# Performance work log

Measured on AMD Instinct MI355X. Metric: run time of the kernel, lower is better.

The kernel has to match this reference:

```python
import jax, jax.numpy as jnp
import numpy as np

D_IN = 1024
N_HEADS = 16
DEPTH = D_IN // N_HEADS
SCALE = float(np.sqrt(DEPTH))


def setup_inputs() -> dict:
    key = jax.random.key(0)
    ks = jax.random.split(key, 11)
    B, S = 4, 1024
    s = 0.02
    return {
        "q": jax.random.normal(ks[0], (B, S, D_IN), jnp.float32),
        "k": jax.random.normal(ks[1], (B, S, D_IN), jnp.float32),
        "v": jax.random.normal(ks[2], (B, S, D_IN), jnp.float32),
        "mask": jnp.zeros((1, 1, S, S), jnp.float32),
        "wq_w": jax.random.normal(ks[3], (D_IN, D_IN), jnp.float32) * s,
        "wq_b": jax.random.normal(ks[4], (D_IN,), jnp.float32) * s,
        "wk_w": jax.random.normal(ks[5], (D_IN, D_IN), jnp.float32) * s,
        "wk_b": jax.random.normal(ks[6], (D_IN,), jnp.float32) * s,
        "wv_w": jax.random.normal(ks[7], (D_IN, D_IN), jnp.float32) * s,
        "wv_b": jax.random.normal(ks[8], (D_IN,), jnp.float32) * s,
        "pl_w": jax.random.normal(ks[9], (D_IN, D_IN), jnp.float32) * s,
        "pl_b": jax.random.normal(ks[10], (D_IN,), jnp.float32) * s,
    }


def _split_heads(x):
    # [B, S, D] -> [B, H, S, depth]
    B, S, _ = x.shape
    return x.reshape(B, S, N_HEADS, DEPTH).transpose(0, 2, 1, 3)


def reference(q, k, v, mask, wq_w, wq_b, wk_w, wk_b, wv_w, wv_b, pl_w, pl_b):
    # torch Linear: y = x @ W.T + b
    qh = _split_heads(q @ wq_w.T + wq_b)
    kh = _split_heads(k @ wk_w.T + wk_b)
    vh = _split_heads(v @ wv_w.T + wv_b)
    # [B, H, Sq, Sk]
    logits = jnp.einsum("bhqd,bhkd->bhqk", qh, kh) / SCALE
    logits = logits + mask * (-1e9)
    weights = jax.nn.softmax(logits, axis=-1)
    attn = jnp.einsum("bhqk,bhkd->bhqd", weights, vh)
    B = q.shape[0]
    attn = attn.transpose(0, 2, 1, 3).reshape(B, -1, D_IN)
    return attn @ pl_w.T + pl_b
```

## Files before the change

### kernel.cpp

```cpp
#include <hip/hip_runtime.h>
#include <stdint.h>

#define B_ 4
#define S_ 1024
#define DMODEL 1024
#define H_ 16
#define DP_ 64

typedef __attribute__((ext_vector_type(8))) short short8;
typedef __attribute__((ext_vector_type(4))) float floatx4;
typedef __attribute__((ext_vector_type(16))) float floatx16;
typedef __attribute__((ext_vector_type(8))) unsigned short ushort8;
typedef __attribute__((ext_vector_type(4))) unsigned short ushort4v;

#define LOG2E 1.44269504088896f

__device__ __forceinline__ unsigned short f2bf(float x) {
    union { float f; unsigned int u; } c; c.f = x;
    unsigned int r = c.u + 0x7FFFu + ((c.u >> 16) & 1u);
    return (unsigned short)(r >> 16);
}
__device__ __forceinline__ unsigned short f2bf_fast(float x) {
    union { float f; unsigned int u; } c; c.f = x;
    return (unsigned short)((c.u + 0x8000u) >> 16);
}
__device__ __forceinline__ float bf2f(unsigned short b) {
    union { float f; unsigned int u; } c; c.u = ((unsigned int)b) << 16;
    return c.f;
}

#if __has_builtin(__builtin_amdgcn_exp2f)
#define EXP2(x) __builtin_amdgcn_exp2f(x)
#else
#define EXP2(x) exp2f(x)
#endif

#define GLDS16(gp, lp) __builtin_amdgcn_global_load_lds( \
    (const __attribute__((address_space(1))) void*)(gp),  \
    (__attribute__((address_space(3))) void*)(lp), 16, 0, 0)

__global__ __launch_bounds__(256) void convert_all(
    const float* __restrict__ q, const float* __restrict__ k, const float* __restrict__ v,
    const float* __restrict__ wq, const float* __restrict__ wk, const float* __restrict__ wv,
    const float* __restrict__ wp, const float* __restrict__ mask,
    unsigned short* __restrict__ ws)
{
    const unsigned g = blockIdx.x * 256u + threadIdx.x;
    const float* s; unsigned short* d; unsigned off; float sc = 1.0f;
    if (g < 524288u)        { s = q;  d = ws;            off = g; }
    else if (g < 1048576u)  { s = k;  d = ws + 4194304;  off = g - 524288u; }
    else if (g < 1572864u)  { s = v;  d = ws + 8388608;  off = g - 1048576u; }
    else if (g < 1703936u)  { s = wq; d = ws + 12582912; off = g - 1572864u; }
    else if (g < 1835008u)  { s = wk; d = ws + 13631488; off = g - 1703936u; }
    else if (g < 1966080u)  { s = wv; d = ws + 14680064; off = g - 1835008u; }
    else if (g < 2097152u)  { s = wp; d = ws + 15728640; off = g - 1966080u; }
    else { s = mask; d = ws + 16777216; off = g - 2097152u; sc = -1e9f * LOG2E; }
    const floatx4 a = ((const floatx4*)s)[(size_t)off * 2];
    const floatx4 b = ((const floatx4*)s)[(size_t)off * 2 + 1];
    ushort8 r;
    r[0] = f2bf(a[0] * sc); r[1] = f2bf(a[1] * sc); r[2] = f2bf(a[2] * sc); r[3] = f2bf(a[3] * sc);
    r[4] = f2bf(b[0] * sc); r[5] = f2bf(b[1] * sc); r[6] = f2bf(b[2] * sc); r[7] = f2bf(b[3] * sc);
    ((ushort8*)d)[off] = r;
}

template<bool SWAP>
__device__ __forceinline__ void gemm_body(
    const unsigned short* __restrict__ X, const unsigned short* __restrict__ W,
    const int row0, const int col0,
    unsigned short* Xs, unsigned short* Ws, floatx4* acc)
{
    const int tid = threadIdx.x, w = tid >> 6, lane = tid & 63;
    const int l15 = lane & 15, l4 = lane >> 4;
    const int wr = w >> 1, wc = w & 1;
    const int srow = lane >> 3;
    const int sgrp = (lane & 7) ^ srow;
    auto* XsL = (__attribute__((address_space(3))) unsigned short*)Xs;
    auto* WsL = (__attribute__((address_space(3))) unsigned short*)Ws;

    for (int it = 0; it < 16; it++) {
        const int kk = it * 64;
        __syncthreads();
        for (int j = 0; j < 4; j++) {
            const int rb = w * 32 + j * 8;
            GLDS16(X + (size_t)(row0 + rb + srow) * DMODEL + kk + sgrp * 8, XsL + rb * 64);
            GLDS16(W + (size_t)(col0 + rb + srow) * DMODEL + kk + sgrp * 8, WsL + rb * 64);
        }
        __syncthreads();
        for (int ks = 0; ks < 2; ks++) {
            const int slot = ((ks * 4 + l4) ^ (l15 & 7)) * 8;
            short8 xf[4], wf[4];
            for (int t = 0; t < 4; t++) {
                xf[t] = *(const short8*)(Xs + (wr * 64 + t * 16 + l15) * 64 + slot);
                wf[t] = *(const short8*)(Ws + (wc * 64 + t * 16 + l15) * 64 + slot);
            }
            for (int a = 0; a < 4; a++)
                for (int b2 = 0; b2 < 4; b2++)
                    acc[a * 4 + b2] = SWAP
                        ? __builtin_amdgcn_mfma_f32_16x16x32_bf16(wf[a], xf[b2], acc[a * 4 + b2], 0, 0, 0)
                        : __builtin_amdgcn_mfma_f32_16x16x32_bf16(xf[a], wf[b2], acc[a * 4 + b2], 0, 0, 0);
        }
    }
}

__global__ __launch_bounds__(256, 3) void qkv_gemm(
    const unsigned short* __restrict__ Xall, const unsigned short* __restrict__ Wall,
    const float* __restrict__ bq, const float* __restrict__ bk, const float* __restrict__ bv,
    unsigned short* __restrict__ Qh, unsigned short* __restrict__ Kh,
    unsigned short* __restrict__ Vt)
{
    __shared__ unsigned short Xs[8192];
    __shared__ unsigned short Ws[8192];
    const int sel = blockIdx.y >> 5;
    const int row0 = (blockIdx.y & 31) * 128, col0 = blockIdx.x * 128;
    const unsigned short* X = Xall + (size_t)sel * 4194304;
    const unsigned short* W = Wall + (size_t)sel * 1048576;
    const float* bias = (sel == 0) ? bq : (sel == 1) ? bk : bv;

    const int tid = threadIdx.x, w = tid >> 6, lane = tid & 63;
    const int l15 = lane & 15, l4 = lane >> 4;
    const int wr = w >> 1, wc = w & 1;

    floatx4 acc[16];
    for (int i = 0; i < 16; i++) acc[i] = (floatx4){0.f, 0.f, 0.f, 0.f};

    if (sel < 2) {
        gemm_body<true>(X, W, row0, col0, Xs, Ws, acc);
        unsigned short* Out = sel ? Kh : Qh;
        const float scale = sel ? 1.0f : 0.125f * LOG2E;
        for (int nt = 0; nt < 4; nt++) {
            const int n0 = col0 + wc * 64 + nt * 16 + l4 * 4;
            const floatx4 bv4 = *(const floatx4*)(bias + n0);
            const int h = n0 >> 6, d0 = n0 & 63;
            for (int mt = 0; mt < 4; mt++) {
                const int m = row0 + wr * 64 + mt * 16 + l15;
                const int b = m >> 10, s = m & 1023;
                const floatx4 a = acc[nt * 4 + mt];
                ushort4v pk;
                for (int i = 0; i < 4; i++) pk[i] = f2bf((a[i] + bv4[i]) * scale);
                *(ushort4v*)(Out + (((size_t)(b * H_ + h) * S_ + s) * DP_ + d0)) = pk;
            }
        }
    } else {
        gemm_body<false>(X, W, row0, col0, Xs, Ws, acc);
        for (int mt = 0; mt < 4; mt++) {
            const int m0 = row0 + wr * 64 + mt * 16 + l4 * 4;
            const int b = m0 >> 10, s0 = m0 & 1023;
            for (int nt = 0; nt < 4; nt++) {
                const int n = col0 + wc * 64 + nt * 16 + l15;
                const int h = n >> 6, d = n & 63;
                const float bvv = bias[n];
                const floatx4 a = acc[mt * 4 + nt];
                ushort4v pk;
                for (int i = 0; i < 4; i++) pk[i] = f2bf(a[i] + bvv);
                *(ushort4v*)(Vt + (((size_t)(b * H_ + h) * DP_ + d) * S_ + s0)) = pk;
            }
        }
    }
}

__global__ __launch_bounds__(256, 4) void out_gemm(
    const unsigned short* __restrict__ X, const unsigned short* __restrict__ W,
    const float* __restrict__ bias, float* __restrict__ Out)
{
    __shared__ unsigned short Xs[128 * 64];
    __shared__ unsigned short Ws[64 * 64];
    const int row0 = blockIdx.y * 128, col0 = blockIdx.x * 64;
    const int tid = threadIdx.x, w = tid >> 6, lane = tid & 63;
    const int l15 = lane & 15, l4 = lane >> 4;
    const int srow = lane >> 3, sgrp = (lane & 7) ^ srow;
    auto* XsL = (__attribute__((address_space(3))) unsigned short*)Xs;
    auto* WsL = (__attribute__((address_space(3))) unsigned short*)Ws;

    floatx4 acc[8];
    for (int i = 0; i < 8; i++) acc[i] = (floatx4){0.f, 0.f, 0.f, 0.f};

    for (int it = 0; it < 16; it++) {
        const int kk = it * 64;
        __syncthreads();
        for (int j = 0; j < 4; j++) {
            const int rb = w * 32 + j * 8;
            GLDS16(X + (size_t)(row0 + rb + srow) * DMODEL + kk + sgrp * 8, XsL + rb * 64);
        }
        for (int j = 0; j < 2; j++) {
            const int rb = w * 16 + j * 8;
            GLDS16(W + (size_t)(col0 + rb + srow) * DMODEL + kk + sgrp * 8, WsL + rb * 64);
        }
        __syncthreads();
        for (int ks = 0; ks < 2; ks++) {
            const int slot = ((ks * 4 + l4) ^ (l15 & 7)) * 8;
            short8 xf[2], wf[4];
            for (int t = 0; t < 2; t++)
                xf[t] = *(const short8*)(Xs + (w * 32 + t * 16 + l15) * 64 + slot);
            for (int t = 0; t < 4; t++)
                wf[t] = *(const short8*)(Ws + (t * 16 + l15) * 64 + slot);
            for (int nt = 0; nt < 4; nt++)
                for (int mt = 0; mt < 2; mt++)
                    acc[nt * 2 + mt] = __builtin_amdgcn_mfma_f32_16x16x32_bf16(
                        wf[nt], xf[mt], acc[nt * 2 + mt], 0, 0, 0);
        }
    }

    for (int nt = 0; nt < 4; nt++) {
        const int n0 = col0 + nt * 16 + l4 * 4;
        const floatx4 bv4 = *(const floatx4*)(bias + n0);
        for (int mt = 0; mt < 2; mt++) {
            const int m = row0 + w * 32 + mt * 16 + l15;
            floatx4 ov;
            for (int i = 0; i < 4; i++) ov[i] = acc[nt * 2 + mt][i] + bv4[i];
            *(floatx4*)(Out + (size_t)m * DMODEL + n0) = ov;
        }
    }
}

__global__ __launch_bounds__(256, 3) void attn_fwd(
    const unsigned short* __restrict__ Qh, const unsigned short* __restrict__ Kh,
    const unsigned short* __restrict__ Vt, const unsigned short* __restrict__ maskb,
    unsigned short* __restrict__ attnO)
{
    __shared__ unsigned short Ks[2 * 4096];
    __shared__ unsigned short Vs[2 * 4096];
    __shared__ unsigned short Ps[2 * 2048];
    auto* KsL = (__attribute__((address_space(3))) unsigned short*)Ks;
    auto* VsL = (__attribute__((address_space(3))) unsigned short*)Vs;

    const int bh = blockIdx.x, qt = blockIdx.y;
    const int b = bh >> 4, h = bh & 15;
    const int tid = threadIdx.x, w = tid >> 6, lane = tid & 63;
    const int l31 = lane & 31, hh = lane >> 5;
    const int qh = w >> 1, kh = w & 1;
    const int srow = lane >> 3, sgrp = (lane & 7) ^ srow;
    unsigned short* PsQ = Ps + qh * 2048;
    const int qg = qt * 64 + qh * 32 + l31;
    const int sw7 = l31 & 7;

    short8 bq[4];
    for (int c = 0; c < 4; c++)
        bq[c] = *(const short8*)(Qh + ((size_t)bh * S_ + qg) * DP_ + c * 16 + hh * 8);

    for (int j = 0; j < 2; j++) {
        const int rb = w * 16 + j * 8;
        GLDS16(Kh + ((size_t)bh * S_ + rb + srow) * DP_ + sgrp * 8, KsL + rb * 64);
        GLDS16(Vt + ((size_t)bh * DP_ + rb + srow) * S_ + sgrp * 8, VsL + rb * 64);
    }
    ushort4v mk[4], mkn[4];
    for (int rq = 0; rq < 4; rq++)
        mk[rq] = *(const ushort4v*)(maskb + (size_t)qg * S_ + kh * 32 + rq * 8 + hh * 4);

    float l_i = 0.f;
    floatx16 o;
    for (int i = 0; i < 16; i++) o[i] = 0.f;

    for (int kt = 0; kt < 16; kt++) {
        const int cur = kt & 1, nxt = cur ^ 1;
        __syncthreads();
        if (kt < 15) {
            for (int j = 0; j < 2; j++) {
                const int rb = w * 16 + j * 8;
                GLDS16(Kh + ((size_t)bh * S_ + (kt + 1) * 64 + rb + srow) * DP_ + sgrp * 8,
                       KsL + nxt * 4096 + rb * 64);
            }
            for (int rq = 0; rq < 4; rq++)
                mkn[rq] = *(const ushort4v*)(maskb + (size_t)qg * S_ + (kt + 1) * 64 + kh * 32 + rq * 8 + hh * 4);
        }

        const unsigned short* Kc = Ks + cur * 4096;
        floatx16 sa;
        for (int i = 0; i < 16; i++) sa[i] = 0.f;
        for (int c = 0; c < 4; c++) {
            short8 ak = *(const short8*)(Kc + (kh * 32 + l31) * 64 + ((c * 2 + hh) ^ sw7) * 8);
            sa = __builtin_amdgcn_mfma_f32_32x32x16_bf16(ak, bq[c], sa, 0, 0, 0);
        }

        for (int rq = 0; rq < 4; rq++) {
            ushort4v pk;
            for (int i = 0; i < 4; i++) {
                const float p = EXP2(sa[rq * 4 + i] + bf2f(mk[rq][i]));
                l_i += p;
                pk[i] = f2bf_fast(p);
            }
            *(ushort4v*)(PsQ + l31 * 64 + ((kh * 4 + rq) ^ sw7) * 8 + hh * 4) = pk;
        }
        __syncthreads();
        if (kt < 15) {
            for (int j = 0; j < 2; j++) {
                const int rb = w * 16 + j * 8;
                GLDS16(Vt + ((size_t)bh * DP_ + rb + srow) * S_ + (kt + 1) * 64 + sgrp * 8,
                       VsL + nxt * 4096 + rb * 64);
            }
        }

        const unsigned short* Vc = Vs + cur * 4096;
        for (int c2 = 0; c2 < 4; c2++) {
            short8 av = *(const short8*)(Vc + (kh * 32 + l31) * 64 + ((c2 * 2 + hh) ^ sw7) * 8);
            short8 bp = *(const short8*)(PsQ + l31 * 64 + ((c2 * 2 + hh) ^ sw7) * 8);
            o = __builtin_amdgcn_mfma_f32_32x32x16_bf16(av, bp, o, 0, 0, 0);
        }

        if (kt < 15)
            for (int rq = 0; rq < 4; rq++) mk[rq] = mkn[rq];
    }

    __syncthreads();
    l_i += __shfl_xor(l_i, 32, 64);
    float* Lbuf = (float*)Ks;
    if (lane < 32) Lbuf[w * 32 + l31] = l_i;
    __syncthreads();
    const float inv = 1.0f / (Lbuf[qh * 64 + l31] + Lbuf[qh * 64 + 32 + l31]);

    unsigned short* T = Ks + 1024;
    for (int rq = 0; rq < 4; rq++) {
        ushort4v pk;
        for (int i = 0; i < 4; i++) pk[i] = f2bf(o[rq * 4 + i] * inv);
        const int qq = qh * 32 + l31;
        *(ushort4v*)(T + qq * 64 + ((kh * 4 + rq) ^ sw7) * 8 + hh * 4) = pk;
    }
    __syncthreads();
    const int r = tid >> 2;
    for (int t = 0; t < 2; t++) {
        const int g = (tid & 3) + t * 4;
        ushort8 ov = *(const ushort8*)(T + r * 64 + ((g ^ (r & 7)) * 8));
        *(ushort8*)(attnO + ((size_t)(b * S_ + qt * 64 + r)) * DMODEL + h * DP_ + g * 8) = ov;
    }
}

extern "C" void kernel_launch(void* const* d_in, const int* in_sizes, int n_in,
                              void* d_out, int out_size, void* d_ws, size_t ws_size,
                              hipStream_t stream)
{
    (void)in_sizes; (void)n_in; (void)out_size; (void)ws_size;
    const float* q    = (const float*)d_in[0];
    const float* k    = (const float*)d_in[1];
    const float* v    = (const float*)d_in[2];
    const float* mask = (const float*)d_in[3];
    const float* wq_w = (const float*)d_in[4];
    const float* wq_b = (const float*)d_in[5];
    const float* wk_w = (const float*)d_in[6];
    const float* wk_b = (const float*)d_in[7];
    const float* wv_w = (const float*)d_in[8];
    const float* wv_b = (const float*)d_in[9];
    const float* pl_w = (const float*)d_in[10];
    const float* pl_b = (const float*)d_in[11];

    unsigned short* ws = (unsigned short*)d_ws;
    unsigned short* Xall  = ws;
    unsigned short* Wall  = ws + 12582912;
    unsigned short* Wp    = ws + 15728640;
    unsigned short* maskb = ws + 16777216;
    unsigned short* Qh    = ws + 17825792;
    unsigned short* Kh    = ws + 22020096;
    unsigned short* Vt    = ws + 4194304;
    unsigned short* attnB = ws;

    dim3 bb(256, 1, 1);
    convert_all<<<dim3(8704, 1, 1), bb, 0, stream>>>(q, k, v, wq_w, wk_w, wv_w, pl_w, mask, ws);
    qkv_gemm<<<dim3(8, 96, 1), bb, 0, stream>>>(Xall, Wall, wq_b, wk_b, wv_b, Qh, Kh, Vt);
    attn_fwd<<<dim3(64, 16, 1), bb, 0, stream>>>(Qh, Kh, Vt, maskb, attnB);
    out_gemm<<<dim3(16, 32, 1), bb, 0, stream>>>(attnB, Wp, pl_b, (float*)d_out);
}
```

Baseline: 220.1 us.

## Keep P in registers via lane shuffles and split PV over key halves

The attention kernel stops writing the softmax probabilities to shared memory and reading them back. Each wave packs its P values to bf16 and swaps halves with the partner lane using cross-lane shuffles to build the PV MFMA operand directly. Each wave now computes all 64 output dims over its own 32-key half, and the two key-half partial outputs are combined through shared memory in the epilogue. This removes the Ps buffer and the mid-iteration barrier, moves the V prefetch to the top of the loop, and raises the occupancy hint to 4; the cost is twice the output accumulator registers and an extra reduction step.

```diff
diff --git a/kernel.cpp b/kernel.cpp
--- a/kernel.cpp
+++ b/kernel.cpp
@@ -12,6 +12,7 @@
 typedef __attribute__((ext_vector_type(16))) float floatx16;
 typedef __attribute__((ext_vector_type(8))) unsigned short ushort8;
 typedef __attribute__((ext_vector_type(4))) unsigned short ushort4v;
+typedef __attribute__((ext_vector_type(4))) unsigned int uintx4;
 
 #define LOG2E 1.44269504088896f
 
@@ -20,13 +21,13 @@
     unsigned int r = c.u + 0x7FFFu + ((c.u >> 16) & 1u);
     return (unsigned short)(r >> 16);
 }
-__device__ __forceinline__ unsigned short f2bf_fast(float x) {
-    union { float f; unsigned int u; } c; c.f = x;
-    return (unsigned short)((c.u + 0x8000u) >> 16);
-}
 __device__ __forceinline__ float bf2f(unsigned short b) {
     union { float f; unsigned int u; } c; c.u = ((unsigned int)b) << 16;
     return c.f;
+}
+__device__ __forceinline__ unsigned pack2(float lo, float hi) {
+    union { float f; unsigned int u; } a, b; a.f = lo; b.f = hi;
+    return ((b.u + 0x8000u) & 0xFFFF0000u) | ((a.u + 0x8000u) >> 16);
 }
 
 #if __has_builtin(__builtin_amdgcn_exp2f)
@@ -212,14 +213,13 @@
     }
 }
 
-__global__ __launch_bounds__(256, 3) void attn_fwd(
+__global__ __launch_bounds__(256, 4) void attn_fwd(
     const unsigned short* __restrict__ Qh, const unsigned short* __restrict__ Kh,
     const unsigned short* __restrict__ Vt, const unsigned short* __restrict__ maskb,
     unsigned short* __restrict__ attnO)
 {
     __shared__ unsigned short Ks[2 * 4096];
     __shared__ unsigned short Vs[2 * 4096];
-    __shared__ unsigned short Ps[2 * 2048];
     auto* KsL = (__attribute__((address_space(3))) unsigned short*)Ks;
     auto* VsL = (__attribute__((address_space(3))) unsigned short*)Vs;
 
@@ -229,7 +229,6 @@
     const int l31 = lane & 31, hh = lane >> 5;
     const int qh = w >> 1, kh = w & 1;
     const int srow = lane >> 3, sgrp = (lane & 7) ^ srow;
-    unsigned short* PsQ = Ps + qh * 2048;
     const int qg = qt * 64 + qh * 32 + l31;
     const int sw7 = l31 & 7;
 
@@ -243,12 +242,13 @@
         GLDS16(Vt + ((size_t)bh * DP_ + rb + srow) * S_ + sgrp * 8, VsL + rb * 64);
     }
     ushort4v mk[4], mkn[4];
-    for (int rq = 0; rq < 4; rq++)
-        mk[rq] = *(const ushort4v*)(maskb + (size_t)qg * S_ + kh * 32 + rq * 8 + hh * 4);
+    for (int t = 0; t < 4; t++)
+        mk[t] = *(const ushort4v*)(maskb + (size_t)qg * S_ + kh * 32 + t * 8 + hh * 4);
 
     float l_i = 0.f;
-    floatx16 o;
-    for (int i = 0; i < 16; i++) o[i] = 0.f;
+    floatx16 o[2];
+    for (int du = 0; du < 2; du++)
+        for (int i = 0; i < 16; i++) o[du][i] = 0.f;
 
     for (int kt = 0; kt < 16; kt++) {
         const int cur = kt & 1, nxt = cur ^ 1;
@@ -258,12 +258,15 @@
                 const int rb = w * 16 + j * 8;
                 GLDS16(Kh + ((size_t)bh * S_ + (kt + 1) * 64 + rb + srow) * DP_ + sgrp * 8,
                        KsL + nxt * 4096 + rb * 64);
-            }
-            for (int rq = 0; rq < 4; rq++)
-                mkn[rq] = *(const ushort4v*)(maskb + (size_t)qg * S_ + (kt + 1) * 64 + kh * 32 + rq * 8 + hh * 4);
+                GLDS16(Vt + ((size_t)bh * DP_ + rb + srow) * S_ + (kt + 1) * 64 + sgrp * 8,
+                       VsL + nxt * 4096 + rb * 64);
+            }
+            for (int t = 0; t < 4; t++)
+                mkn[t] = *(const ushort4v*)(maskb + (size_t)qg * S_ + (kt + 1) * 64 + kh * 32 + t * 8 + hh * 4);
         }
 
         const unsigned short* Kc = Ks + cur * 4096;
+        const unsigned short* Vc = Vs + cur * 4096;
         floatx16 sa;
         for (int i = 0; i < 16; i++) sa[i] = 0.f;
         for (int c = 0; c < 4; c++) {
@@ -271,48 +274,71 @@
             sa = __builtin_amdgcn_mfma_f32_32x32x16_bf16(ak, bq[c], sa, 0, 0, 0);
         }
 
-        for (int rq = 0; rq < 4; rq++) {
-            ushort4v pk;
-            for (int i = 0; i < 4; i++) {
-                const float p = EXP2(sa[rq * 4 + i] + bf2f(mk[rq][i]));
-                l_i += p;
-                pk[i] = f2bf_fast(p);
-            }
-            *(ushort4v*)(PsQ + l31 * 64 + ((kh * 4 + rq) ^ sw7) * 8 + hh * 4) = pk;
-        }
-        __syncthreads();
-        if (kt < 15) {
-            for (int j = 0; j < 2; j++) {
-                const int rb = w * 16 + j * 8;
-                GLDS16(Vt + ((size_t)bh * DP_ + rb + srow) * S_ + (kt + 1) * 64 + sgrp * 8,
-                       VsL + nxt * 4096 + rb * 64);
-            }
-        }
-
-        const unsigned short* Vc = Vs + cur * 4096;
-        for (int c2 = 0; c2 < 4; c2++) {
-            short8 av = *(const short8*)(Vc + (kh * 32 + l31) * 64 + ((c2 * 2 + hh) ^ sw7) * 8);
-            short8 bp = *(const short8*)(PsQ + l31 * 64 + ((c2 * 2 + hh) ^ sw7) * 8);
-            o = __builtin_amdgcn_mfma_f32_32x32x16_bf16(av, bp, o, 0, 0, 0);
-        }
+        unsigned pd[8];
+        for (int t = 0; t < 4; t++) {
+            float p0 = EXP2(sa[t * 4 + 0] + bf2f(mk[t][0]));
+            float p1 = EXP2(sa[t * 4 + 1] + bf2f(mk[t][1]));
+            float p2 = EXP2(sa[t * 4 + 2] + bf2f(mk[t][2]));
+            float p3 = EXP2(sa[t * 4 + 3] + bf2f(mk[t][3]));
+            l_i += (p0 + p1) + (p2 + p3);
+            pd[t * 2 + 0] = pack2(p0, p1);
+            pd[t * 2 + 1] = pack2(p2, p3);
+        }
+
+        unsigned snd0 = hh ? pd[0] : pd[2];
+        unsigned snd1 = hh ? pd[1] : pd[3];
+        unsigned snd2 = hh ? pd[4] : pd[6];
+        unsigned snd3 = hh ? pd[5] : pd[7];
+        unsigned r0 = (unsigned)__shfl_xor((int)snd0, 32, 64);
+        unsigned r1 = (unsigned)__shfl_xor((int)snd1, 32, 64);
+        unsigned r2 = (unsigned)__shfl_xor((int)snd2, 32, 64);
+        unsigned r3 = (unsigned)__shfl_xor((int)snd3, 32, 64);
+        uintx4 u0 = { hh ? r0 : pd[0], hh ? r1 : pd[1], hh ? pd[2] : r0, hh ? pd[3] : r1 };
+        uintx4 u1 = { hh ? r2 : pd[4], hh ? r3 : pd[5], hh ? pd[6] : r2, hh ? pd[7] : r3 };
+        short8 bp[2];
+        bp[0] = __builtin_bit_cast(short8, u0);
+        bp[1] = __builtin_bit_cast(short8, u1);
+
+        for (int c2 = 0; c2 < 2; c2++)
+            for (int du = 0; du < 2; du++) {
+                short8 av = *(const short8*)(Vc + (du * 32 + l31) * 64 + ((kh * 4 + c2 * 2 + hh) ^ sw7) * 8);
+                o[du] = __builtin_amdgcn_mfma_f32_32x32x16_bf16(av, bp[c2], o[du], 0, 0, 0);
+            }
 
         if (kt < 15)
-            for (int rq = 0; rq < 4; rq++) mk[rq] = mkn[rq];
+            for (int t = 0; t < 4; t++) mk[t] = mkn[t];
     }
 
     __syncthreads();
     l_i += __shfl_xor(l_i, 32, 64);
-    float* Lbuf = (float*)Ks;
+    float* Lbuf = (float*)(Vs + 4096);
     if (lane < 32) Lbuf[w * 32 + l31] = l_i;
+
+    float* Obuf = (float*)Ks;
+    if (kh == 1) {
+        for (int du = 0; du < 2; du++)
+            for (int rr = 0; rr < 4; rr++) {
+                floatx4 v4 = { o[du][rr * 4 + 0], o[du][rr * 4 + 1],
+                               o[du][rr * 4 + 2], o[du][rr * 4 + 3] };
+                *(floatx4*)(Obuf + qh * 2048 + l31 * 64 +
+                            ((du * 8 + rr * 2 + hh) ^ (l31 & 15)) * 4) = v4;
+            }
+    }
     __syncthreads();
-    const float inv = 1.0f / (Lbuf[qh * 64 + l31] + Lbuf[qh * 64 + 32 + l31]);
-
-    unsigned short* T = Ks + 1024;
-    for (int rq = 0; rq < 4; rq++) {
-        ushort4v pk;
-        for (int i = 0; i < 4; i++) pk[i] = f2bf(o[rq * 4 + i] * inv);
-        const int qq = qh * 32 + l31;
-        *(ushort4v*)(T + qq * 64 + ((kh * 4 + rq) ^ sw7) * 8 + hh * 4) = pk;
+
+    unsigned short* T = Vs;
+    if (kh == 0) {
+        const float inv = 1.0f / (Lbuf[(qh * 2) * 32 + l31] + Lbuf[(qh * 2 + 1) * 32 + l31]);
+        for (int du = 0; du < 2; du++)
+            for (int rr = 0; rr < 4; rr++) {
+                floatx4 part = *(const floatx4*)(Obuf + qh * 2048 + l31 * 64 +
+                                ((du * 8 + rr * 2 + hh) ^ (l31 & 15)) * 4);
+                ushort4v pk;
+                for (int i = 0; i < 4; i++)
+                    pk[i] = f2bf((o[du][rr * 4 + i] + part[i]) * inv);
+                *(ushort4v*)(T + (qh * 32 + l31) * 64 +
+                             ((du * 4 + rr) ^ sw7) * 8 + hh * 4) = pk;
+            }
     }
     __syncthreads();
     const int r = tid >> 2;
```

New measurement: 224.7 us. 1.02x slower.
